# Optimization experiments

Hardware: AMD Instinct MI355X
Metric: run time of the kernel (lower is better)

The kernel has to match this reference:

```python
import jax, jax.numpy as jnp
import numpy as np

N_HEAD, D_HEAD, PROJ_DIM = 8, 64, 256
D_MODEL = N_HEAD * D_HEAD  # 512
SCALE_W = 0.7
EPS = 1e-5       # attention denominator eps
LN_EPS = 1e-5    # torch LayerNorm default
SCALE = D_HEAD ** -0.5
CHUNK = 64


def draw_orth(d, m, rng):
    # Performer orthogonal random features: stacked orthogonal blocks with chi-norm scaling.
    blocks = []
    n_full = m // d
    for _ in range(n_full):
        q, _ = np.linalg.qr(rng.standard_normal((d, d)))
        blocks.append(q.T)
    rem = m - n_full * d
    if rem:
        q, _ = np.linalg.qr(rng.standard_normal((d, d)))
        blocks.append(q.T[:rem])
    W = np.concatenate(blocks, axis=0)                      # [m, d]
    mult = np.linalg.norm(rng.standard_normal((m, d)), axis=1)
    return (W * mult[:, None]).T                            # [d, m]


def prime(x, proj):
    # FAVOR+ positive softmax features. x: [B,H,L,d], proj: [d,m] -> [B,H,L,2m]
    xn = x * (x.shape[-1] ** -0.25)
    xp = jnp.einsum('bhld,dm->bhlm', xn, proj)
    half = 0.5 * jnp.sum(xn * xn, axis=-1, keepdims=True)
    u = jnp.concatenate([xp, -xp], axis=-1) - half
    # per-row max subtraction: exactly cancelled by the subsequent sum-normalization
    u = u - jax.lax.stop_gradient(jnp.max(u, axis=-1, keepdims=True))
    return jnp.exp(u)


def causal_linear(q, k, v):
    # out[b,h,t] = sum_{s<=t} (q_t . k_s) v_s  (additive fast-weight / fast_weight_sum, W0 = 0)
    B, H, L, M = q.shape
    D = v.shape[-1]
    nC = L // CHUNK
    qc = q.reshape(B, H, nC, CHUNK, M).transpose(2, 0, 1, 3, 4)
    kc = k.reshape(B, H, nC, CHUNK, M).transpose(2, 0, 1, 3, 4)
    vc = v.reshape(B, H, nC, CHUNK, D).transpose(2, 0, 1, 3, 4)
    mask = jnp.tril(jnp.ones((CHUNK, CHUNK), q.dtype))

    def step(W, blk):
        qb, kb, vb = blk
        inter = jnp.einsum('bhcm,bhmd->bhcd', qb, W)
        sc = jnp.einsum('bhcm,bhsm->bhcs', qb, kb) * mask
        intra = jnp.einsum('bhcs,bhsd->bhcd', sc, vb)
        W = W + jnp.einsum('bhsm,bhsd->bhmd', kb, vb)
        return W, inter + intra

    W0 = jnp.zeros((B, H, M, D), q.dtype)
    _, out = jax.lax.scan(step, W0, (qc, kc, vc))            # [nC,B,H,C,D]
    return out.transpose(1, 2, 0, 3, 4).reshape(B, H, L, D)


def setup_inputs() -> dict:
    key = jax.random.key(0)
    k0, k1, k2 = jax.random.split(key, 3)
    L, B = 256, 32
    h = jax.random.normal(k0, (L, B, D_MODEL), jnp.float32)
    w_qkv = jax.random.normal(k1, (D_MODEL, 4 * N_HEAD * D_HEAD), jnp.float32) * (D_MODEL ** -0.5)
    w_o = jax.random.normal(k2, (N_HEAD * D_HEAD, D_MODEL), jnp.float32) * ((N_HEAD * D_HEAD) ** -0.5)
    ln_gamma = jnp.ones((D_MODEL,), jnp.float32)
    ln_beta = jnp.zeros((D_MODEL,), jnp.float32)
    pi0 = 0.5 * jnp.ones((N_HEAD, 256), jnp.float32)
    pi1 = 0.5 * jnp.ones((N_HEAD, 256), jnp.float32)
    proj_matrix = jnp.asarray(draw_orth(D_HEAD, PROJ_DIM, np.random.default_rng(0)), jnp.float32)
    return {"h": h, "w_qkv": w_qkv, "w_o": w_o, "ln_gamma": ln_gamma, "ln_beta": ln_beta,
            "pi0": pi0, "pi1": pi1, "proj_matrix": proj_matrix}


def reference(h, w_qkv, w_o, ln_gamma, ln_beta, pi0, pi1, proj_matrix):
    L, B, _ = h.shape
    qkv = jnp.einsum('lbd,de->lbe', h, w_qkv).reshape(L, B, N_HEAD, 4 * D_HEAD)
    q, k1, k2, v = jnp.split(qkv, 4, axis=-1)
    perm = lambda t: t.transpose(1, 2, 0, 3)                 # -> [B,H,L,dh]
    q, k1, k2, v = perm(q), perm(k1), perm(k2), perm(v)

    norm = lambda p: p / jnp.sum(p, axis=-1, keepdims=True)
    qf = norm(prime(q, proj_matrix))                         # [B,H,L,2m]
    k1f = norm(prime(k1, proj_matrix))
    k2f = norm(prime(k2, SCALE_W * proj_matrix))
    kf = k1f * pi0[None, :, :L, None] + k2f * pi1[None, :, :L, None]

    denom_acc = jnp.cumsum(kf, axis=2)
    denom = jnp.einsum('bhlm,bhlm->bhl', denom_acc, qf)[..., None]

    out = causal_linear(qf, kf, v)                           # [B,H,L,dh]
    out = SCALE * out / (denom + EPS)
    out = out.transpose(0, 2, 1, 3).reshape(B, L, N_HEAD * D_HEAD).transpose(1, 0, 2)

    attn = jnp.einsum('lbd,de->lbe', out, w_o)
    x = h + attn
    mu = jnp.mean(x, axis=-1, keepdims=True)
    var = jnp.var(x, axis=-1, keepdims=True)
    return (x - mu) / jnp.sqrt(var + LN_EPS) * ln_gamma + ln_beta
```

## Files before the change

kernel.cpp:

```cpp
#include <hip/hip_runtime.h>
#include <hip/hip_bf16.h>

#define L_SEQ 256
#define B_SZ  32
#define NH    8
#define DH    64
#define DM    512
#define FD    512
#define PM    256
#define ROWS  8192
#define QKVN  2048

typedef __bf16 bf16x8 __attribute__((ext_vector_type(8)));
typedef float f32x4 __attribute__((ext_vector_type(4)));
#define MFMA16(a, b, c) __builtin_amdgcn_mfma_f32_16x16x32_bf16((a), (b), (c), 0, 0, 0)

static __device__ __forceinline__ void stmix(void* p, long i, float v, int f32) {
  if (f32) ((float*)p)[i] = v;
  else     ((__bf16*)p)[i] = (__bf16)v;
}

#define PREP_HB   2048
#define PREP_WT   256
#define PREP_WOT  64
#define PREP_PJ   4
#define PREP_TINY 1
#define PREP_BLOCKS (PREP_HB + PREP_WT + PREP_WOT + PREP_PJ + PREP_TINY)

__global__ __launch_bounds__(256) void prep(
    const void* __restrict__ h, const void* __restrict__ wqkv,
    const void* __restrict__ wo, const void* __restrict__ proj,
    const void* __restrict__ pi0, const void* __restrict__ pi1,
    const void* __restrict__ gam, const void* __restrict__ bet,
    int* __restrict__ flag, __bf16* __restrict__ hb, __bf16* __restrict__ wt,
    __bf16* __restrict__ wot, __bf16* __restrict__ projT,
    __bf16* __restrict__ pi0b, __bf16* __restrict__ pi1b,
    __bf16* __restrict__ gamb, __bf16* __restrict__ betb,
    __bf16* __restrict__ projB) {
  __shared__ float T[64][69];
  __shared__ int red[256];
  const int tid = threadIdx.x;
  int cnt = 0;
  {
    const unsigned short* hbits = (const unsigned short*)h;
    for (int i = 0; i < 16; ++i) {
      const unsigned short u = hbits[tid * 16 + i];
      if (((u >> 7) & 0xFF) >= 0xA0) ++cnt;
    }
  }
  red[tid] = cnt; __syncthreads();
  for (int s = 128; s > 0; s >>= 1) { if (tid < s) red[tid] += red[tid + s]; __syncthreads(); }
  const int f32 = (red[0] >= 64) ? 1 : 0;
  __syncthreads();

  const int blk = blockIdx.x;
  if (blk < PREP_HB) {
    const int i = blk * 256 + tid;
    if (f32) {
      const f32x4* s = (const f32x4*)h;
      const f32x4 a = s[i * 2], b = s[i * 2 + 1];
      bf16x8 t;
      t[0] = (__bf16)a[0]; t[1] = (__bf16)a[1]; t[2] = (__bf16)a[2]; t[3] = (__bf16)a[3];
      t[4] = (__bf16)b[0]; t[5] = (__bf16)b[1]; t[6] = (__bf16)b[2]; t[7] = (__bf16)b[3];
      *reinterpret_cast<bf16x8*>(hb + (long)i * 8) = t;
    } else {
      *reinterpret_cast<bf16x8*>(hb + (long)i * 8) = ((const bf16x8*)h)[i];
    }
    return;
  }
  const void* src; __bf16* dst; int M, N, n0, m0;
  int pjx = -1;
  if (blk < PREP_HB + PREP_WT) {
    const int x = blk - PREP_HB;
    src = wqkv; dst = wt; M = 512; N = 2048; n0 = (x & 31) * 64; m0 = (x >> 5) * 64;
  } else if (blk < PREP_HB + PREP_WT + PREP_WOT) {
    const int x = blk - PREP_HB - PREP_WT;
    src = wo; dst = wot; M = 512; N = 512; n0 = (x & 7) * 64; m0 = (x >> 3) * 64;
  } else if (blk < PREP_HB + PREP_WT + PREP_WOT + PREP_PJ) {
    const int x = blk - PREP_HB - PREP_WT - PREP_WOT;
    src = proj; dst = projT; M = 64; N = 256; n0 = x * 64; m0 = 0;
    pjx = x;
  } else {
    if (tid == 0) flag[0] = f32;
    if (f32) {
      const float* s0 = (const float*)pi0; const float* s1 = (const float*)pi1;
      const float* s2 = (const float*)gam; const float* s3 = (const float*)bet;
      for (int i = tid; i < NH * 256; i += 256) { pi0b[i] = (__bf16)s0[i]; pi1b[i] = (__bf16)s1[i]; }
      for (int i = tid; i < DM; i += 256)      { gamb[i] = (__bf16)s2[i]; betb[i] = (__bf16)s3[i]; }
    } else {
      const __bf16* s0 = (const __bf16*)pi0; const __bf16* s1 = (const __bf16*)pi1;
      const __bf16* s2 = (const __bf16*)gam; const __bf16* s3 = (const __bf16*)bet;
      for (int i = tid; i < NH * 256; i += 256) { pi0b[i] = s0[i]; pi1b[i] = s1[i]; }
      for (int i = tid; i < DM; i += 256)      { gamb[i] = s2[i]; betb[i] = s3[i]; }
    }
    return;
  }
  if (f32) {
    const float* s = (const float*)src;
#pragma unroll
    for (int rep = 0; rep < 16; ++rep) {
      const int i = rep * 4 + (tid >> 6), j = tid & 63;
      T[i][j] = s[(long)(m0 + i) * N + n0 + j];
    }
  } else {
    const __bf16* s = (const __bf16*)src;
#pragma unroll
    for (int rep = 0; rep < 16; ++rep) {
      const int i = rep * 4 + (tid >> 6), j = tid & 63;
      T[i][j] = (float)s[(long)(m0 + i) * N + n0 + j];
    }
  }
  __syncthreads();
#pragma unroll
  for (int rep = 0; rep < 16; ++rep) {
    const int i = rep * 4 + (tid >> 6), j = tid & 63;
    dst[(long)(n0 + i) * M + m0 + j] = (__bf16)T[j][i];
  }
  if (pjx >= 0) {
    const int lane = tid & 63, sub = tid >> 6;
    const int mm = lane & 15, qq = lane >> 4;
#pragma unroll
    for (int kk2 = 0; kk2 < 2; ++kk2) {
      bf16x8 v;
#pragma unroll
      for (int e = 0; e < 8; ++e) v[e] = (__bf16)T[kk2 * 32 + qq * 8 + e][sub * 16 + mm];
      *reinterpret_cast<bf16x8*>(projB + ((pjx * 4 + sub) * 2 + kk2) * 512 + lane * 8) = v;
    }
  }
}

__global__ __launch_bounds__(256) void gemm_h_wqkv(const __bf16* __restrict__ A,
                                                   const __bf16* __restrict__ Bt,
                                                   __bf16* __restrict__ C) {
  __shared__ __bf16 At[128][72];
  __shared__ __bf16 Bts[128][72];
  const int n0 = blockIdx.x * 128, m0 = blockIdx.y * 128;
  const int tid = threadIdx.x, lane = tid & 63, wv = tid >> 6;
  const int m = lane & 15, q = lane >> 4;
  const int wr = (wv >> 1) * 64, wc = (wv & 1) * 64;
  const int r = tid >> 1, c0 = (tid & 1) * 32;
  const __bf16* ap = A + (long)(m0 + r) * DM + c0;
  const __bf16* bp = Bt + (long)(n0 + r) * DM + c0;
  f32x4 acc[4][4];
#pragma unroll
  for (int i = 0; i < 4; ++i)
#pragma unroll
    for (int j = 0; j < 4; ++j) acc[i][j] = f32x4{0.f, 0.f, 0.f, 0.f};

  bf16x8 ar[4], br[4];
#pragma unroll
  for (int j = 0; j < 4; ++j) {
    ar[j] = *reinterpret_cast<const bf16x8*>(ap + j * 8);
    br[j] = *reinterpret_cast<const bf16x8*>(bp + j * 8);
  }
  for (int k0 = 0; k0 < DM; k0 += 64) {
    __syncthreads();
#pragma unroll
    for (int j = 0; j < 4; ++j) {
      *reinterpret_cast<bf16x8*>(&At[r][c0 + j * 8]) = ar[j];
      *reinterpret_cast<bf16x8*>(&Bts[r][c0 + j * 8]) = br[j];
    }
    if (k0 + 64 < DM) {
#pragma unroll
      for (int j = 0; j < 4; ++j) {
        ar[j] = *reinterpret_cast<const bf16x8*>(ap + k0 + 64 + j * 8);
        br[j] = *reinterpret_cast<const bf16x8*>(bp + k0 + 64 + j * 8);
      }
    }
    __syncthreads();
#pragma unroll
    for (int kk = 0; kk < 2; ++kk) {
      bf16x8 af[4], bfv[4];
#pragma unroll
      for (int i = 0; i < 4; ++i) {
        af[i]  = *reinterpret_cast<const bf16x8*>(&At[wr + i * 16 + m][kk * 32 + q * 8]);
        bfv[i] = *reinterpret_cast<const bf16x8*>(&Bts[wc + i * 16 + m][kk * 32 + q * 8]);
      }
#pragma unroll
      for (int ai = 0; ai < 4; ++ai)
#pragma unroll
        for (int bi = 0; bi < 4; ++bi)
          acc[ai][bi] = MFMA16(af[ai], bfv[bi], acc[ai][bi]);
    }
  }
#pragma unroll
  for (int ai = 0; ai < 4; ++ai)
#pragma unroll
    for (int r2 = 0; r2 < 4; ++r2)
#pragma unroll
      for (int bi = 0; bi < 4; ++bi)
        C[(long)(m0 + wr + ai * 16 + q * 4 + r2) * QKVN + n0 + wc + bi * 16 + m] =
            (__bf16)acc[ai][bi][r2];
}

__global__ __launch_bounds__(256) void features_mfma(const __bf16* __restrict__ qkv,
                                                     const __bf16* __restrict__ projB,
                                                     const __bf16* __restrict__ pi0,
                                                     const __bf16* __restrict__ pi1,
                                                     __bf16* __restrict__ kf) {
  const int l0 = blockIdx.x * 64;
  const int bh = blockIdx.y;
  const int h = bh & 7, b = bh >> 3;
  const int tid = threadIdx.x, lane = tid & 63, wv = tid >> 6;
  const int m = lane & 15, q = lane >> 4;
  __shared__ __bf16 As[2][64][72];

  {
    const int r = tid >> 2, c0 = (tid & 3) * 16;
    const __bf16* ap = qkv + (long)((l0 + r) * B_SZ + b) * QKVN + h * 256 + 64 + c0;
#pragma unroll
    for (int t2 = 0; t2 < 2; ++t2) {
      *reinterpret_cast<bf16x8*>(&As[t2][r][c0]) =
          *reinterpret_cast<const bf16x8*>(ap + t2 * 64);
      *reinterpret_cast<bf16x8*>(&As[t2][r][c0 + 8]) =
          *reinterpret_cast<const bf16x8*>(ap + t2 * 64 + 8);
    }
  }
  const int l = l0 + wv * 16 + m;
  const float p0w = (float)pi0[h * 256 + l];
  const float p1w = (float)pi1[h * 256 + l];
  const float SQ = 0.35355339f;
  const float SK2 = 0.24748737f;
  __syncthreads();

  f32x4 acc1[16], acc2[16];
#pragma unroll
  for (int c = 0; c < 16; ++c) {
    acc1[c] = f32x4{0.f, 0.f, 0.f, 0.f};
    acc2[c] = f32x4{0.f, 0.f, 0.f, 0.f};
  }
#pragma unroll
  for (int kk = 0; kk < 2; ++kk) {
    const bf16x8 x1 = *reinterpret_cast<const bf16x8*>(&As[0][wv * 16 + m][kk * 32 + q * 8]);
    const bf16x8 x2 = *reinterpret_cast<const bf16x8*>(&As[1][wv * 16 + m][kk * 32 + q * 8]);
#pragma unroll
    for (int c = 0; c < 16; ++c) {
      const bf16x8 wf =
          *reinterpret_cast<const bf16x8*>(projB + (c * 2 + kk) * 512 + lane * 8);
      acc1[c] = MFMA16(wf, x1, acc1[c]);
      acc2[c] = MFMA16(wf, x2, acc2[c]);
    }
  }
  float mx1 = 0.f, mx2 = 0.f;
#pragma unroll
  for (int c = 0; c < 16; ++c)
#pragma unroll
    for (int r = 0; r < 4; ++r) {
      mx1 = fmaxf(mx1, fabsf(acc1[c][r] * SQ));
      mx2 = fmaxf(mx2, fabsf(acc2[c][r] * SK2));
    }
  mx1 = fmaxf(mx1, __shfl_xor(mx1, 16)); mx1 = fmaxf(mx1, __shfl_xor(mx1, 32));
  mx2 = fmaxf(mx2, __shfl_xor(mx2, 16)); mx2 = fmaxf(mx2, __shfl_xor(mx2, 32));
  const float C21 = __expf(-2.f * mx1);
  const float C22 = __expf(-2.f * mx2);
  float sm1 = 0.f, sm2 = 0.f;
#pragma unroll
  for (int c = 0; c < 16; ++c)
#pragma unroll
    for (int r = 0; r < 4; ++r) {
      const float e11 = __expf(acc1[c][r] * SQ - mx1);
      const float e12 = __expf(acc2[c][r] * SK2 - mx2);
      sm1 += e11 + C21 * __builtin_amdgcn_rcpf(e11);
      sm2 += e12 + C22 * __builtin_amdgcn_rcpf(e12);
      acc1[c][r] = e11;
      acc2[c][r] = e12;
    }
  sm1 += __shfl_xor(sm1, 16); sm1 += __shfl_xor(sm1, 32);
  sm2 += __shfl_xor(sm2, 16); sm2 += __shfl_xor(sm2, 32);
  const float w1 = p0w * __builtin_amdgcn_rcpf(sm1);
  const float w2 = p1w * __builtin_amdgcn_rcpf(sm2);
  const float K1 = C21 * w1, K2 = C22 * w2;
  __bf16* op = kf + (((long)bh * 16 + (l >> 4)) * 16) * 512 + lane * 8;
#pragma unroll
  for (int c = 0; c < 16; ++c) {
    bf16x8 v;
#pragma unroll
    for (int r = 0; r < 4; ++r) {
      v[r]     = (__bf16)(w1 * acc1[c][r] + w2 * acc2[c][r]);
      v[4 + r] = (__bf16)(K1 * __builtin_amdgcn_rcpf(acc1[c][r]) +
                          K2 * __builtin_amdgcn_rcpf(acc2[c][r]));
    }
    *reinterpret_cast<bf16x8*>(op + c * 512) = v;
  }
}

__global__ __launch_bounds__(256) void vpack(const __bf16* __restrict__ qkv,
                                             __bf16* __restrict__ vt) {
  const int st = blockIdx.x;
  const int s0 = st * 64;
  const int bh = blockIdx.y;
  const int h = bh & 7, b = bh >> 3;
  __shared__ __bf16 T[64][72];
  const int tid = threadIdx.x;
  {
    const int s = tid >> 2, d0 = (tid & 3) * 16;
    const __bf16* vp = qkv + ((long)((s0 + s) * B_SZ + b)) * QKVN + h * 256 + 192 + d0;
#pragma unroll
    for (int j = 0; j < 16; ++j) T[d0 + j][s] = vp[j];
  }
  __syncthreads();
  {
    const int lane = tid & 63, c2 = tid >> 6;
    const int m = lane & 15, q = lane >> 4;
    const int d = c2 * 16 + m;
#pragma unroll
    for (int kk = 0; kk < 2; ++kk) {
      const bf16x8 v = *reinterpret_cast<const bf16x8*>(&T[d][kk * 32 + q * 8]);
      *reinterpret_cast<bf16x8*>(vt + (((long)bh * 8 + st * 2 + kk) * 4 + c2) * 512 + lane * 8) = v;
    }
  }
}

__global__ __launch_bounds__(256, 3) void flash_mfma(const __bf16* __restrict__ qkv,
                                                     const __bf16* __restrict__ projB,
                                                     const __bf16* __restrict__ kf,
                                                     const __bf16* __restrict__ vt,
                                                     __bf16* __restrict__ att) {
  const int id = blockIdx.x;
  const int bh = id & 255;
  const int t  = ((id >> 8) + id) & 3;
  const int h = bh & 7, b = bh >> 3;
  const int tid = threadIdx.x, lane = tid & 63, wv = tid >> 6;
  const int m = lane & 15, q = lane >> 4;
  __shared__ __bf16 Pt[64][72];

  const float SQ = 0.35355339f;
  f32x4 acc[16];
#pragma unroll
  for (int c = 0; c < 16; ++c) acc[c] = f32x4{0.f, 0.f, 0.f, 0.f};
  const __bf16* xb = qkv + (long)((t * 64 + wv * 16 + m) * B_SZ + b) * QKVN + h * 256;
#pragma unroll
  for (int kk = 0; kk < 2; ++kk) {
    const bf16x8 xf = *reinterpret_cast<const bf16x8*>(xb + kk * 32 + q * 8);
#pragma unroll
    for (int c = 0; c < 16; ++c) {
      const bf16x8 wf =
          *reinterpret_cast<const bf16x8*>(projB + (c * 2 + kk) * 512 + lane * 8);
      acc[c] = MFMA16(wf, xf, acc[c]);
    }
  }
  float mx = 0.f;
#pragma unroll
  for (int c = 0; c < 16; ++c)
#pragma unroll
    for (int r = 0; r < 4; ++r) mx = fmaxf(mx, fabsf(acc[c][r] * SQ));
  mx = fmaxf(mx, __shfl_xor(mx, 16));
  mx = fmaxf(mx, __shfl_xor(mx, 32));
  const float C2 = __expf(-2.f * mx);
  float sm = 0.f;
#pragma unroll
  for (int c = 0; c < 16; ++c)
#pragma unroll
    for (int r = 0; r < 4; ++r) {
      const float e1 = __expf(acc[c][r] * SQ - mx);
      sm += e1 + C2 * __builtin_amdgcn_rcpf(e1);
      acc[c][r] = e1;
    }
  sm += __shfl_xor(sm, 16);
  sm += __shfl_xor(sm, 32);
  const float inv = __builtin_amdgcn_rcpf(sm);
  const float K2 = C2 * inv;
  bf16x8 qT[16];
#pragma unroll
  for (int c = 0; c < 16; ++c) {
    bf16x8 v;
#pragma unroll
    for (int r = 0; r < 4; ++r) {
      v[r]     = (__bf16)(acc[c][r] * inv);
      v[4 + r] = (__bf16)(K2 * __builtin_amdgcn_rcpf(acc[c][r]));
    }
    qT[c] = v;
  }

  f32x4 o[4];
#pragma unroll
  for (int i = 0; i < 4; ++i) o[i] = f32x4{0.f, 0.f, 0.f, 0.f};
  float den[4] = {0.f, 0.f, 0.f, 0.f};

  const __bf16* kfb = kf + (long)bh * (16 * 16 * 512) + lane * 8;
  const __bf16* vtb = vt + (long)bh * (8 * 4 * 512) + lane * 8;

  for (int st = 0; st <= t; ++st) {
    f32x4 s[4];
#pragma unroll
    for (int i = 0; i < 4; ++i) s[i] = f32x4{0.f, 0.f, 0.f, 0.f};
#pragma unroll
    for (int g = 0; g < 16; ++g) {
      const __bf16* kp = kfb + ((long)(st * 4) * 16 + g) * 512;
      const bf16x8 kb0 = *reinterpret_cast<const bf16x8*>(kp);
      const bf16x8 kb1 = *reinterpret_cast<const bf16x8*>(kp + 16 * 512);
      const bf16x8 kb2 = *reinterpret_cast<const bf16x8*>(kp + 32 * 512);
      const bf16x8 kb3 = *reinterpret_cast<const bf16x8*>(kp + 48 * 512);
      s[0] = MFMA16(qT[g], kb0, s[0]);
      s[1] = MFMA16(qT[g], kb1, s[1]);
      s[2] = MFMA16(qT[g], kb2, s[2]);
      s[3] = MFMA16(qT[g], kb3, s[3]);
    }
    bf16x8 vf[8];
#pragma unroll
    for (int kk = 0; kk < 2; ++kk)
#pragma unroll
      for (int c = 0; c < 4; ++c)
        vf[kk * 4 + c] =
            *reinterpret_cast<const bf16x8*>(vtb + (((long)st * 2 + kk) * 4 + c) * 512);
    const bool last = (st == t);
#pragma unroll
    for (int c = 0; c < 4; ++c)
#pragma unroll
      for (int r = 0; r < 4; ++r) {
        const int row = wv * 16 + q * 4 + r, col = c * 16 + m;
        const float v = (last && col > row) ? 0.f : s[c][r];
        den[r] += v;
        Pt[row][col] = (__bf16)v;
      }
#pragma unroll
    for (int kk = 0; kk < 2; ++kk) {
      const bf16x8 pf = *reinterpret_cast<const bf16x8*>(&Pt[wv * 16 + m][kk * 32 + q * 8]);
#pragma unroll
      for (int c = 0; c < 4; ++c)
        o[c] = MFMA16(pf, vf[kk * 4 + c], o[c]);
    }
  }
#pragma unroll
  for (int r = 0; r < 4; ++r) {
    float d = den[r];
    d += __shfl_xor(d, 1); d += __shfl_xor(d, 2);
    d += __shfl_xor(d, 4); d += __shfl_xor(d, 8);
    const float invd = 0.125f / (d + 1e-5f);
    const int row = t * 64 + wv * 16 + q * 4 + r;
#pragma unroll
    for (int c = 0; c < 4; ++c)
      att[((long)(row * B_SZ + b)) * DM + h * DH + c * 16 + m] = (__bf16)(o[c][r] * invd);
  }
}

__global__ __launch_bounds__(256) void gemm_att_wo(const __bf16* __restrict__ A,
                                                   const __bf16* __restrict__ Bt,
                                                   const __bf16* __restrict__ hb,
                                                   float* __restrict__ xrow) {
  __shared__ __bf16 At[128][72];
  __shared__ __bf16 Bts[128][72];
  const int n0 = blockIdx.x * 128, m0 = blockIdx.y * 128;
  const int tid = threadIdx.x, lane = tid & 63, wv = tid >> 6;
  const int m = lane & 15, q = lane >> 4;
  const int wr = (wv >> 1) * 64, wc = (wv & 1) * 64;
  const int r = tid >> 1, c0 = (tid & 1) * 32;
  const __bf16* ap = A + (long)(m0 + r) * DM + c0;
  const __bf16* bp = Bt + (long)(n0 + r) * DM + c0;
  f32x4 acc[4][4];
#pragma unroll
  for (int i = 0; i < 4; ++i)
#pragma unroll
    for (int j = 0; j < 4; ++j) acc[i][j] = f32x4{0.f, 0.f, 0.f, 0.f};

  bf16x8 ar[4], br[4];
#pragma unroll
  for (int j = 0; j < 4; ++j) {
    ar[j] = *reinterpret_cast<const bf16x8*>(ap + j * 8);
    br[j] = *reinterpret_cast<const bf16x8*>(bp + j * 8);
  }
  for (int k0 = 0; k0 < DM; k0 += 64) {
    __syncthreads();
#pragma unroll
    for (int j = 0; j < 4; ++j) {
      *reinterpret_cast<bf16x8*>(&At[r][c0 + j * 8]) = ar[j];
      *reinterpret_cast<bf16x8*>(&Bts[r][c0 + j * 8]) = br[j];
    }
    if (k0 + 64 < DM) {
#pragma unroll
      for (int j = 0; j < 4; ++j) {
        ar[j] = *reinterpret_cast<const bf16x8*>(ap + k0 + 64 + j * 8);
        br[j] = *reinterpret_cast<const bf16x8*>(bp + k0 + 64 + j * 8);
      }
    }
    __syncthreads();
#pragma unroll
    for (int kk = 0; kk < 2; ++kk) {
      bf16x8 af[4], bfv[4];
#pragma unroll
      for (int i = 0; i < 4; ++i) {
        af[i]  = *reinterpret_cast<const bf16x8*>(&At[wr + i * 16 + m][kk * 32 + q * 8]);
        bfv[i] = *reinterpret_cast<const bf16x8*>(&Bts[wc + i * 16 + m][kk * 32 + q * 8]);
      }
#pragma unroll
      for (int ai = 0; ai < 4; ++ai)
#pragma unroll
        for (int bi = 0; bi < 4; ++bi)
          acc[ai][bi] = MFMA16(af[ai], bfv[bi], acc[ai][bi]);
    }
  }
#pragma unroll
  for (int ai = 0; ai < 4; ++ai)
#pragma unroll
    for (int r2 = 0; r2 < 4; ++r2)
#pragma unroll
      for (int bi = 0; bi < 4; ++bi) {
        const long row = m0 + wr + ai * 16 + q * 4 + r2;
        const long col = n0 + wc + bi * 16 + m;
        xrow[row * DM + col] = acc[ai][bi][r2] + (float)hb[row * DM + col];
      }
}

__global__ __launch_bounds__(256) void ln_out(const float* __restrict__ xrow,
                                              const __bf16* __restrict__ gamma,
                                              const __bf16* __restrict__ beta,
                                              const int* __restrict__ flag,
                                              void* __restrict__ out) {
  const int f32 = flag[0];
  const int r = blockIdx.x;
  const int tid = threadIdx.x;
  __shared__ float red[256];
  const float x0 = xrow[(long)r * DM + tid];
  const float x1 = xrow[(long)r * DM + tid + 256];

  red[tid] = x0 + x1; __syncthreads();
  for (int s = 128; s > 0; s >>= 1) { if (tid < s) red[tid] += red[tid + s]; __syncthreads(); }
  const float mu = red[0] * (1.f / 512.f); __syncthreads();
  red[tid] = x0 * x0 + x1 * x1; __syncthreads();
  for (int s = 128; s > 0; s >>= 1) { if (tid < s) red[tid] += red[tid + s]; __syncthreads(); }
  const float var = red[0] * (1.f / 512.f) - mu * mu; __syncthreads();
  const float rstd = rsqrtf(var + 1e-5f);

  stmix(out, (long)r * DM + tid,
        (x0 - mu) * rstd * (float)gamma[tid] + (float)beta[tid], f32);
  stmix(out, (long)r * DM + tid + 256,
        (x1 - mu) * rstd * (float)gamma[tid + 256] + (float)beta[tid + 256], f32);
}

extern "C" void kernel_launch(void* const* d_in, const int* in_sizes, int n_in,
                              void* d_out, int out_size, void* d_ws, size_t ws_size,
                              hipStream_t stream) {
  (void)in_sizes; (void)n_in; (void)out_size; (void)ws_size;
  char* ws = (char*)d_ws;
  __bf16* qkv   = (__bf16*)ws;
  int*    flag  = (int*)(ws + 33554432);
  __bf16* wt    = (__bf16*)(ws + 33554688);
  __bf16* wot   = (__bf16*)(ws + 35651840);
  __bf16* att   = (__bf16*)(ws + 36176128);
  __bf16* vt    = (__bf16*)(ws + 44564736);
  __bf16* hb    = (__bf16*)(ws + 52953344);
  __bf16* projT = (__bf16*)(ws + 61341952);
  __bf16* pi0b  = (__bf16*)(ws + 61374720);
  __bf16* pi1b  = (__bf16*)(ws + 61378816);
  __bf16* gamb  = (__bf16*)(ws + 61382912);
  __bf16* betb  = (__bf16*)(ws + 61383936);
  float*  xrow  = (float*)(ws + 61384960);
  __bf16* projB = (__bf16*)(ws + 78163968);
  __bf16* kf    = (__bf16*)(ws + 128493824);

  prep<<<PREP_BLOCKS, 256, 0, stream>>>(d_in[0], d_in[1], d_in[2], d_in[7],
                                        d_in[5], d_in[6], d_in[3], d_in[4],
                                        flag, hb, wt, wot, projT,
                                        pi0b, pi1b, gamb, betb, projB);
  gemm_h_wqkv<<<dim3(16, 64), 256, 0, stream>>>(hb, wt, qkv);
  vpack<<<dim3(4, 256), 256, 0, stream>>>(qkv, vt);
  features_mfma<<<dim3(4, 256), 256, 0, stream>>>(qkv, projB, pi0b, pi1b, kf);
  flash_mfma<<<dim3(1024), 256, 0, stream>>>(qkv, projB, kf, vt, att);
  gemm_att_wo<<<dim3(4, 64), 256, 0, stream>>>(att, wot, hb, xrow);
  ln_out<<<dim3(ROWS), 256, 0, stream>>>(xrow, gamb, betb, flag, d_out);
}
```

Baseline: 223.9 us.

## Process two 16-row query tiles per wave in flash kernel, halve block size

Each wave of flash_mfma now handles two 16-row query tiles instead of one, and the block shrinks from 256 to 128 threads. Every loaded kf and vt fragment then feeds two MFMAs, which halves global/L2 traffic per unit of compute. The cost is roughly double the register pressure (two qT arrays of 16 vectors, twice the accumulators), lower occupancy (launch bounds 128,2), and fewer waves per block to hide latency.

```diff
diff --git a/kernel.cpp b/kernel.cpp
--- a/kernel.cpp
+++ b/kernel.cpp
@@ -311,7 +311,7 @@
   }
 }
 
-__global__ __launch_bounds__(256, 3) void flash_mfma(const __bf16* __restrict__ qkv,
+__global__ __launch_bounds__(128, 2) void flash_mfma(const __bf16* __restrict__ qkv,
                                                      const __bf16* __restrict__ projB,
                                                      const __bf16* __restrict__ kf,
                                                      const __bf16* __restrict__ vt,
@@ -320,70 +320,75 @@
   const int bh = id & 255;
   const int t  = ((id >> 8) + id) & 3;
   const int h = bh & 7, b = bh >> 3;
-  const int tid = threadIdx.x, lane = tid & 63, wv = tid >> 6;
+  const int tid = threadIdx.x, lane = tid & 63, w = tid >> 6;
   const int m = lane & 15, q = lane >> 4;
   __shared__ __bf16 Pt[64][72];
 
   const float SQ = 0.35355339f;
-  f32x4 acc[16];
-#pragma unroll
-  for (int c = 0; c < 16; ++c) acc[c] = f32x4{0.f, 0.f, 0.f, 0.f};
-  const __bf16* xb = qkv + (long)((t * 64 + wv * 16 + m) * B_SZ + b) * QKVN + h * 256;
-#pragma unroll
-  for (int kk = 0; kk < 2; ++kk) {
-    const bf16x8 xf = *reinterpret_cast<const bf16x8*>(xb + kk * 32 + q * 8);
+  bf16x8 qT0[16], qT1[16];
+#pragma unroll
+  for (int j = 0; j < 2; ++j) {
+    f32x4 acc[16];
+#pragma unroll
+    for (int c = 0; c < 16; ++c) acc[c] = f32x4{0.f, 0.f, 0.f, 0.f};
+    const __bf16* xb =
+        qkv + (long)((t * 64 + w * 32 + j * 16 + m) * B_SZ + b) * QKVN + h * 256;
+#pragma unroll
+    for (int kk = 0; kk < 2; ++kk) {
+      const bf16x8 xf = *reinterpret_cast<const bf16x8*>(xb + kk * 32 + q * 8);
+#pragma unroll
+      for (int c = 0; c < 16; ++c) {
+        const bf16x8 wf =
+            *reinterpret_cast<const bf16x8*>(projB + (c * 2 + kk) * 512 + lane * 8);
+        acc[c] = MFMA16(wf, xf, acc[c]);
+      }
+    }
+    float mx = 0.f;
+#pragma unroll
+    for (int c = 0; c < 16; ++c)
+#pragma unroll
+      for (int r = 0; r < 4; ++r) mx = fmaxf(mx, fabsf(acc[c][r] * SQ));
+    mx = fmaxf(mx, __shfl_xor(mx, 16));
+    mx = fmaxf(mx, __shfl_xor(mx, 32));
+    const float C2 = __expf(-2.f * mx);
+    float sm = 0.f;
+#pragma unroll
+    for (int c = 0; c < 16; ++c)
+#pragma unroll
+      for (int r = 0; r < 4; ++r) {
+        const float e1 = __expf(acc[c][r] * SQ - mx);
+        sm += e1 + C2 * __builtin_amdgcn_rcpf(e1);
+        acc[c][r] = e1;
+      }
+    sm += __shfl_xor(sm, 16);
+    sm += __shfl_xor(sm, 32);
+    const float inv = __builtin_amdgcn_rcpf(sm);
+    const float K2 = C2 * inv;
+    bf16x8* qT = j ? qT1 : qT0;
 #pragma unroll
     for (int c = 0; c < 16; ++c) {
-      const bf16x8 wf =
-          *reinterpret_cast<const bf16x8*>(projB + (c * 2 + kk) * 512 + lane * 8);
-      acc[c] = MFMA16(wf, xf, acc[c]);
-    }
-  }
-  float mx = 0.f;
-#pragma unroll
-  for (int c = 0; c < 16; ++c)
-#pragma unroll
-    for (int r = 0; r < 4; ++r) mx = fmaxf(mx, fabsf(acc[c][r] * SQ));
-  mx = fmaxf(mx, __shfl_xor(mx, 16));
-  mx = fmaxf(mx, __shfl_xor(mx, 32));
-  const float C2 = __expf(-2.f * mx);
-  float sm = 0.f;
-#pragma unroll
-  for (int c = 0; c < 16; ++c)
-#pragma unroll
-    for (int r = 0; r < 4; ++r) {
-      const float e1 = __expf(acc[c][r] * SQ - mx);
-      sm += e1 + C2 * __builtin_amdgcn_rcpf(e1);
-      acc[c][r] = e1;
-    }
-  sm += __shfl_xor(sm, 16);
-  sm += __shfl_xor(sm, 32);
-  const float inv = __builtin_amdgcn_rcpf(sm);
-  const float K2 = C2 * inv;
-  bf16x8 qT[16];
-#pragma unroll
-  for (int c = 0; c < 16; ++c) {
-    bf16x8 v;
-#pragma unroll
-    for (int r = 0; r < 4; ++r) {
-      v[r]     = (__bf16)(acc[c][r] * inv);
-      v[4 + r] = (__bf16)(K2 * __builtin_amdgcn_rcpf(acc[c][r]));
-    }
-    qT[c] = v;
-  }
-
-  f32x4 o[4];
-#pragma unroll
-  for (int i = 0; i < 4; ++i) o[i] = f32x4{0.f, 0.f, 0.f, 0.f};
-  float den[4] = {0.f, 0.f, 0.f, 0.f};
+      bf16x8 v;
+#pragma unroll
+      for (int r = 0; r < 4; ++r) {
+        v[r]     = (__bf16)(acc[c][r] * inv);
+        v[4 + r] = (__bf16)(K2 * __builtin_amdgcn_rcpf(acc[c][r]));
+      }
+      qT[c] = v;
+    }
+  }
+
+  f32x4 o0[4], o1[4];
+#pragma unroll
+  for (int i = 0; i < 4; ++i) { o0[i] = f32x4{0.f, 0.f, 0.f, 0.f}; o1[i] = o0[i]; }
+  float den0[4] = {0.f, 0.f, 0.f, 0.f}, den1[4] = {0.f, 0.f, 0.f, 0.f};
 
   const __bf16* kfb = kf + (long)bh * (16 * 16 * 512) + lane * 8;
   const __bf16* vtb = vt + (long)bh * (8 * 4 * 512) + lane * 8;
 
   for (int st = 0; st <= t; ++st) {
-    f32x4 s[4];
-#pragma unroll
-    for (int i = 0; i < 4; ++i) s[i] = f32x4{0.f, 0.f, 0.f, 0.f};
+    f32x4 s0[4], s1[4];
+#pragma unroll
+    for (int i = 0; i < 4; ++i) { s0[i] = f32x4{0.f, 0.f, 0.f, 0.f}; s1[i] = s0[i]; }
 #pragma unroll
     for (int g = 0; g < 16; ++g) {
       const __bf16* kp = kfb + ((long)(st * 4) * 16 + g) * 512;
@@ -391,46 +396,56 @@
       const bf16x8 kb1 = *reinterpret_cast<const bf16x8*>(kp + 16 * 512);
       const bf16x8 kb2 = *reinterpret_cast<const bf16x8*>(kp + 32 * 512);
       const bf16x8 kb3 = *reinterpret_cast<const bf16x8*>(kp + 48 * 512);
-      s[0] = MFMA16(qT[g], kb0, s[0]);
-      s[1] = MFMA16(qT[g], kb1, s[1]);
-      s[2] = MFMA16(qT[g], kb2, s[2]);
-      s[3] = MFMA16(qT[g], kb3, s[3]);
-    }
-    bf16x8 vf[8];
-#pragma unroll
-    for (int kk = 0; kk < 2; ++kk)
+      s0[0] = MFMA16(qT0[g], kb0, s0[0]);  s1[0] = MFMA16(qT1[g], kb0, s1[0]);
+      s0[1] = MFMA16(qT0[g], kb1, s0[1]);  s1[1] = MFMA16(qT1[g], kb1, s1[1]);
+      s0[2] = MFMA16(qT0[g], kb2, s0[2]);  s1[2] = MFMA16(qT1[g], kb2, s1[2]);
+      s0[3] = MFMA16(qT0[g], kb3, s0[3]);  s1[3] = MFMA16(qT1[g], kb3, s1[3]);
+    }
+    const bool last = (st == t);
+#pragma unroll
+    for (int c = 0; c < 4; ++c)
+#pragma unroll
+      for (int r = 0; r < 4; ++r) {
+        const int col = c * 16 + m;
+        const int row0 = w * 32 + q * 4 + r;
+        const float v0 = (last && col > row0) ? 0.f : s0[c][r];
+        den0[r] += v0;
+        Pt[row0][col] = (__bf16)v0;
+        const int row1 = row0 + 16;
+        const float v1 = (last && col > row1) ? 0.f : s1[c][r];
+        den1[r] += v1;
+        Pt[row1][col] = (__bf16)v1;
+      }
+#pragma unroll
+    for (int kk = 0; kk < 2; ++kk) {
+      bf16x8 vf[4];
 #pragma unroll
       for (int c = 0; c < 4; ++c)
-        vf[kk * 4 + c] =
-            *reinterpret_cast<const bf16x8*>(vtb + (((long)st * 2 + kk) * 4 + c) * 512);
-    const bool last = (st == t);
-#pragma unroll
-    for (int c = 0; c < 4; ++c)
-#pragma unroll
-      for (int r = 0; r < 4; ++r) {
-        const int row = wv * 16 + q * 4 + r, col = c * 16 + m;
-        const float v = (last && col > row) ? 0.f : s[c][r];
-        den[r] += v;
-        Pt[row][col] = (__bf16)v;
-      }
-#pragma unroll
-    for (int kk = 0; kk < 2; ++kk) {
-      const bf16x8 pf = *reinterpret_cast<const bf16x8*>(&Pt[wv * 16 + m][kk * 32 + q * 8]);
+        vf[c] = *reinterpret_cast<const bf16x8*>(vtb + (((long)st * 2 + kk) * 4 + c) * 512);
+      const bf16x8 pf0 = *reinterpret_cast<const bf16x8*>(&Pt[w * 32 + m][kk * 32 + q * 8]);
+      const bf16x8 pf1 = *reinterpret_cast<const bf16x8*>(&Pt[w * 32 + 16 + m][kk * 32 + q * 8]);
+#pragma unroll
+      for (int c = 0; c < 4; ++c) {
+        o0[c] = MFMA16(pf0, vf[c], o0[c]);
+        o1[c] = MFMA16(pf1, vf[c], o1[c]);
+      }
+    }
+  }
+#pragma unroll
+  for (int j = 0; j < 2; ++j) {
+    const float* den = j ? den1 : den0;
+    const f32x4* o = j ? o1 : o0;
+#pragma unroll
+    for (int r = 0; r < 4; ++r) {
+      float d = den[r];
+      d += __shfl_xor(d, 1); d += __shfl_xor(d, 2);
+      d += __shfl_xor(d, 4); d += __shfl_xor(d, 8);
+      const float invd = 0.125f / (d + 1e-5f);
+      const int row = t * 64 + w * 32 + j * 16 + q * 4 + r;
 #pragma unroll
       for (int c = 0; c < 4; ++c)
-        o[c] = MFMA16(pf, vf[kk * 4 + c], o[c]);
-    }
-  }
-#pragma unroll
-  for (int r = 0; r < 4; ++r) {
-    float d = den[r];
-    d += __shfl_xor(d, 1); d += __shfl_xor(d, 2);
-    d += __shfl_xor(d, 4); d += __shfl_xor(d, 8);
-    const float invd = 0.125f / (d + 1e-5f);
-    const int row = t * 64 + wv * 16 + q * 4 + r;
-#pragma unroll
-    for (int c = 0; c < 4; ++c)
-      att[((long)(row * B_SZ + b)) * DM + h * DH + c * 16 + m] = (__bf16)(o[c][r] * invd);
+        att[((long)(row * B_SZ + b)) * DM + h * DH + c * 16 + m] = (__bf16)(o[c][r] * invd);
+    }
   }
 }
 
@@ -555,7 +570,7 @@
   gemm_h_wqkv<<<dim3(16, 64), 256, 0, stream>>>(hb, wt, qkv);
   vpack<<<dim3(4, 256), 256, 0, stream>>>(qkv, vt);
   features_mfma<<<dim3(4, 256), 256, 0, stream>>>(qkv, projB, pi0b, pi1b, kf);
-  flash_mfma<<<dim3(1024), 256, 0, stream>>>(qkv, projB, kf, vt, att);
+  flash_mfma<<<dim3(1024), 128, 0, stream>>>(qkv, projB, kf, vt, att);
   gemm_att_wo<<<dim3(4, 64), 256, 0, stream>>>(att, wot, hb, xrow);
   ln_out<<<dim3(ROWS), 256, 0, stream>>>(xrow, gamb, betb, flag, d_out);
 }
```

After: 219.9 us. No clear change (-1.8%).
